# Kernel tuning notes

Hardware: AMD Instinct MI355X
Metric: run time of the kernel (lower is better)

The kernel has to match this reference:

```python
import jax, jax.numpy as jnp
import numpy as np

C = 64
DQK = C // 8  # query/key channels


def setup_inputs() -> dict:
    key = jax.random.key(0)
    ks = jax.random.split(key, 8)
    B, H, W = 4, 64, 64
    x = jax.random.normal(ks[0], (B, C, H, W), dtype=jnp.float32)
    # 1x1 conv weights stored as (out_ch, in_ch); biases as (out_ch,)
    wq = jax.random.normal(ks[1], (DQK, C), dtype=jnp.float32) * 0.05
    bq = jnp.zeros((DQK,), dtype=jnp.float32)
    wk = jax.random.normal(ks[2], (DQK, C), dtype=jnp.float32) * 0.05
    bk = jnp.zeros((DQK,), dtype=jnp.float32)
    wv = jax.random.normal(ks[3], (C, C), dtype=jnp.float32) * 0.05
    bv = jnp.zeros((C,), dtype=jnp.float32)
    gamma = jnp.zeros((1,), dtype=jnp.float32)
    return {"x": x, "wq": wq, "bq": bq, "wk": wk, "bk": bk,
            "wv": wv, "bv": bv, "gamma": gamma}


def reference(x, wq, bq, wk, bk, wv, bv, gamma):
    B, Cc, H, W = x.shape
    N = H * W
    xf = x.reshape(B, Cc, N)  # (B, C, N)
    # 1x1 convs == channel-wise matmuls
    q = jnp.einsum('oc,bcn->bon', wq, xf) + bq[None, :, None]  # (B, dqk, N)
    k = jnp.einsum('oc,bcn->bon', wk, xf) + bk[None, :, None]  # (B, dqk, N)
    v = jnp.einsum('oc,bcn->bon', wv, xf) + bv[None, :, None]  # (B, C, N)
    # qk = q^T k -> (B, N, N), softmax over last dim
    qk = jnp.einsum('bdn,bdm->bnm', q, k)
    attn = jax.nn.softmax(qk, axis=-1)
    # out = v @ attn^T : out[b,c,i] = sum_j v[b,c,j] * attn[b,i,j]
    out = jnp.einsum('bcj,bij->bci', v, attn)
    out = out.reshape(B, Cc, H, W)
    return gamma * out + x
```

## Files before the change

### kernel.cpp

```cpp
#include <hip/hip_runtime.h>
#include <cmath>

namespace {

constexpr int B = 4;
constexpr int C = 64;
constexpr int N = 4096;
constexpr float LOG2E = 1.4426950408889634f;

typedef __bf16 bf16x8 __attribute__((ext_vector_type(8)));
typedef float f32x16 __attribute__((ext_vector_type(16)));
typedef unsigned short u16;

union B8 {
  int4 i;
  bf16x8 h;
  unsigned int w[4];
};

__device__ inline u16 f2bf(float f) {
  unsigned int u = __float_as_uint(f);
  u += 0x7FFFu + ((u >> 16) & 1u);
  return (u16)(u >> 16);
}

__device__ inline unsigned int cvt_pk_bf16(float lo, float hi) {
  unsigned int r;
  asm("v_cvt_pk_bf16_f32 %0, %1, %2" : "=v"(r) : "v"(lo), "v"(hi));
  return r;
}

__device__ inline float exp2_fast(float x) {
#if __has_builtin(__builtin_amdgcn_exp2f)
  return __builtin_amdgcn_exp2f(x);
#else
  return exp2f(x);
#endif
}

__device__ __host__ inline int sigma4(int j) {
  return (j & 3) | ((j & 4) << 1) | ((j & 8) >> 1);
}

__global__ __launch_bounds__(256) void qkv_kernel(
    const float* __restrict__ x,
    const float* __restrict__ wq, const float* __restrict__ bq,
    const float* __restrict__ wk, const float* __restrict__ bk,
    const float* __restrict__ wv, const float* __restrict__ bv,
    u16* __restrict__ qt, u16* __restrict__ kt, u16* __restrict__ vo) {
  const int bid = blockIdx.x;
  const int xcd = bid & 7;
  const int b = xcd >> 1;
  const int cg = (bid >> 3) & 3;
  const int nt = (xcd & 1) * 32 + (bid >> 5);
  const int t = threadIdx.x;
  const int nn = t & 63;
  const int wid = __builtin_amdgcn_readfirstlane(t >> 6);
  const int n = nt * 64 + nn;
  const float* xb = x + (size_t)b * C * N + n;

  const int c0 = cg * 16 + wid * 4;
  float a0 = bv[c0], a1 = bv[c0 + 1], a2 = bv[c0 + 2], a3 = bv[c0 + 3];

  if (cg == 0) {
    const int o0 = wid * 2;
    float qa0 = bq[o0], qa1 = bq[o0 + 1];
    float ka0 = bk[o0], ka1 = bk[o0 + 1];
    #pragma unroll 8
    for (int c = 0; c < C; ++c) {
      const float xv = xb[(size_t)c * N];
      a0 = fmaf(wv[(c0 + 0) * C + c], xv, a0);
      a1 = fmaf(wv[(c0 + 1) * C + c], xv, a1);
      a2 = fmaf(wv[(c0 + 2) * C + c], xv, a2);
      a3 = fmaf(wv[(c0 + 3) * C + c], xv, a3);
      qa0 = fmaf(wq[o0 * C + c], xv, qa0);
      qa1 = fmaf(wq[(o0 + 1) * C + c], xv, qa1);
      ka0 = fmaf(wk[o0 * C + c], xv, ka0);
      ka1 = fmaf(wk[(o0 + 1) * C + c], xv, ka1);
    }
    const unsigned int qw =
        (unsigned int)f2bf(qa0 * LOG2E) | ((unsigned int)f2bf(qa1 * LOG2E) << 16);
    const unsigned int kw =
        (unsigned int)f2bf(ka0) | ((unsigned int)f2bf(ka1) << 16);
    *reinterpret_cast<unsigned int*>(qt + ((size_t)b * N + n) * 8 + o0) = qw;
    *reinterpret_cast<unsigned int*>(kt + ((size_t)b * N + n) * 8 + o0) = kw;
  } else {
    #pragma unroll 8
    for (int c = 0; c < C; ++c) {
      const float xv = xb[(size_t)c * N];
      a0 = fmaf(wv[(c0 + 0) * C + c], xv, a0);
      a1 = fmaf(wv[(c0 + 1) * C + c], xv, a1);
      a2 = fmaf(wv[(c0 + 2) * C + c], xv, a2);
      a3 = fmaf(wv[(c0 + 3) * C + c], xv, a3);
    }
  }

  const int sj = sigma4(n & 15);
  const size_t tb = ((size_t)b * (N / 16) + (n >> 4)) * (C * 16) + sj;
  vo[tb + (size_t)(c0 + 0) * 16] = f2bf(a0);
  vo[tb + (size_t)(c0 + 1) * 16] = f2bf(a1);
  vo[tb + (size_t)(c0 + 2) * 16] = f2bf(a2);
  vo[tb + (size_t)(c0 + 3) * 16] = f2bf(a3);
}

__global__ __launch_bounds__(512, 4) void attn_kernel(
    const u16* __restrict__ qt, const u16* __restrict__ kt,
    const u16* __restrict__ vv, const float* __restrict__ x,
    const float* __restrict__ gamma, float* __restrict__ out) {
  const int bid = blockIdx.x;
  const int xcd = bid & 7;
  const int b = xcd >> 1;
  const int i0 = ((xcd & 1) * 64 + (bid >> 3)) * 32;
  const int t = threadIdx.x;
  const int lane = t & 63;
  const int w = __builtin_amdgcn_readfirstlane(t >> 6);
  const int il = lane & 31;
  const int hi = lane >> 5;

  __shared__ float l_lds[8][32];
  __shared__ u16 o_lds[8][32][66];

  B8 qf;
  if (hi == 0)
    qf.i = *reinterpret_cast<const int4*>(qt + ((size_t)b * N + i0 + il) * 8);
  else
    qf.i = make_int4(0, 0, 0, 0);

  const u16* kbase = kt + (size_t)b * N * 8 + ((size_t)w * 512 + il) * 8;
  const u16* vbase = vv + (size_t)b * (N / 16) * (C * 16) + il * 16 + hi * 8;

  f32x16 accA, accB, zero16;
  #pragma unroll
  for (int r = 0; r < 16; ++r) { accA[r] = 0.f; accB[r] = 0.f; zero16[r] = 0.f; }
  float lrun = 0.f;

  B8 kfA, va0A, va1A, vb0A, vb1A;
  B8 kfB, va0B, va1B, vb0B, vb1B;

  auto LOAD = [&](int jt, B8& kf, B8& va0, B8& va1, B8& vb0, B8& vb1) {
    kf.i = *reinterpret_cast<const int4*>(kbase + jt * 256);
    const u16* vp = vbase + (size_t)((w * 512 + jt * 32) >> 4) * (C * 16);
    va0.i = *reinterpret_cast<const int4*>(vp);
    va1.i = *reinterpret_cast<const int4*>(vp + 1024);
    vb0.i = *reinterpret_cast<const int4*>(vp + 512);
    vb1.i = *reinterpret_cast<const int4*>(vp + 1536);
  };

  auto COMPUTE = [&](const B8& kf, const B8& va0, const B8& va1, const B8& vb0,
                     const B8& vb1) {
    f32x16 S = __builtin_amdgcn_mfma_f32_32x32x16_bf16(kf.h, qf.h, zero16, 0, 0, 0);
    float p[16];
    #pragma unroll
    for (int r = 0; r < 16; ++r) p[r] = exp2_fast(S[r]);
    const float t0 = (p[0] + p[1]) + (p[2] + p[3]);
    const float t1 = (p[4] + p[5]) + (p[6] + p[7]);
    const float t2 = (p[8] + p[9]) + (p[10] + p[11]);
    const float t3 = (p[12] + p[13]) + (p[14] + p[15]);
    lrun += (t0 + t1) + (t2 + t3);
    B8 pf0, pf1;
    pf0.w[0] = cvt_pk_bf16(p[0], p[1]);
    pf0.w[1] = cvt_pk_bf16(p[2], p[3]);
    pf0.w[2] = cvt_pk_bf16(p[4], p[5]);
    pf0.w[3] = cvt_pk_bf16(p[6], p[7]);
    pf1.w[0] = cvt_pk_bf16(p[8], p[9]);
    pf1.w[1] = cvt_pk_bf16(p[10], p[11]);
    pf1.w[2] = cvt_pk_bf16(p[12], p[13]);
    pf1.w[3] = cvt_pk_bf16(p[14], p[15]);
    accA = __builtin_amdgcn_mfma_f32_32x32x16_bf16(va0.h, pf0.h, accA, 0, 0, 0);
    accA = __builtin_amdgcn_mfma_f32_32x32x16_bf16(va1.h, pf1.h, accA, 0, 0, 0);
    accB = __builtin_amdgcn_mfma_f32_32x32x16_bf16(vb0.h, pf0.h, accB, 0, 0, 0);
    accB = __builtin_amdgcn_mfma_f32_32x32x16_bf16(vb1.h, pf1.h, accB, 0, 0, 0);
  };

  LOAD(0, kfA, va0A, va1A, vb0A, vb1A);
  #pragma unroll 1
  for (int it = 0; it < 8; ++it) {
    LOAD(2 * it + 1, kfB, va0B, va1B, vb0B, vb1B);
    COMPUTE(kfA, va0A, va1A, vb0A, vb1A);
    if (it < 7) LOAD(2 * it + 2, kfA, va0A, va1A, vb0A, vb1A);
    COMPUTE(kfB, va0B, va1B, vb0B, vb1B);
  }

  const float lw = lrun + __shfl_xor(lrun, 32);
  if (hi == 0) l_lds[w][il] = lw;
  #pragma unroll
  for (int r = 0; r < 16; r += 2) {
    const int c = (r & 3) + 8 * (r >> 2) + 4 * hi;
    *reinterpret_cast<unsigned int*>(&o_lds[w][il][c]) =
        cvt_pk_bf16(accA[r], accA[r + 1]);
    *reinterpret_cast<unsigned int*>(&o_lds[w][il][c + 32]) =
        cvt_pk_bf16(accB[r], accB[r + 1]);
  }
  __syncthreads();

  const int i = t & 31;
  float Li = 0.f;
  #pragma unroll
  for (int ww = 0; ww < 8; ++ww) Li += l_lds[ww][i];
  const float ginv = gamma[0] / Li;

  #pragma unroll
  for (int q4 = 0; q4 < 4; ++q4) {
    const int flat = t + q4 * 512;
    const int c = flat >> 5;
    float s = 0.f;
    #pragma unroll
    for (int ww = 0; ww < 8; ++ww)
      s += __uint_as_float((unsigned int)o_lds[ww][i][c] << 16);
    const size_t off = ((size_t)b * C + c) * N + i0 + i;
    out[off] = fmaf(ginv, s, x[off]);
  }
}

}

extern "C" void kernel_launch(void* const* d_in, const int* in_sizes, int n_in,
                              void* d_out, int out_size, void* d_ws, size_t ws_size,
                              hipStream_t stream) {
  const float* x     = (const float*)d_in[0];
  const float* wq    = (const float*)d_in[1];
  const float* bq    = (const float*)d_in[2];
  const float* wk    = (const float*)d_in[3];
  const float* bk    = (const float*)d_in[4];
  const float* wv    = (const float*)d_in[5];
  const float* bv    = (const float*)d_in[6];
  const float* gamma = (const float*)d_in[7];
  float* out = (float*)d_out;

  u16* qt = (u16*)d_ws;
  u16* kt = qt + (size_t)B * N * 8;
  u16* vo = kt + (size_t)B * N * 8;

  qkv_kernel<<<B * 64 * 4, 256, 0, stream>>>(x, wq, bq, wk, bk, wv, bv, qt, kt, vo);
  attn_kernel<<<B * (N / 32), 512, 0, stream>>>(qt, kt, vo, x, gamma, out);
}
```

Measured before the change: 29.52 us.

## Use packed f32 FMA/add and load V just-in-time in attention loop

The QKV projection loop now processes two input channels per step with v_pk_fma_f32 on two-lane accumulators, which are summed at the end. This halves the VALU instruction count and allows vector loads of weights. In the attention kernel, V fragments are loaded inside COMPUTE right after the score MFMA instead of being double-buffered a tile ahead, which cuts live registers. The softmax row-sum also uses packed adds. The risk is that V load latency is now exposed within each tile, hidden only by the exp work and by occupancy.

```diff
diff --git a/kernel.cpp b/kernel.cpp
--- a/kernel.cpp
+++ b/kernel.cpp
@@ -10,6 +10,7 @@
 
 typedef __bf16 bf16x8 __attribute__((ext_vector_type(8)));
 typedef float f32x16 __attribute__((ext_vector_type(16)));
+typedef float f32x2 __attribute__((ext_vector_type(2)));
 typedef unsigned short u16;
 
 union B8 {
@@ -27,6 +28,17 @@
 __device__ inline unsigned int cvt_pk_bf16(float lo, float hi) {
   unsigned int r;
   asm("v_cvt_pk_bf16_f32 %0, %1, %2" : "=v"(r) : "v"(lo), "v"(hi));
+  return r;
+}
+
+__device__ inline f32x2 pk_add(f32x2 a, f32x2 b) {
+  f32x2 r;
+  asm("v_pk_add_f32 %0, %1, %2" : "=v"(r) : "v"(a), "v"(b));
+  return r;
+}
+__device__ inline f32x2 pk_fma(f32x2 a, f32x2 b, f32x2 c) {
+  f32x2 r;
+  asm("v_pk_fma_f32 %0, %1, %2, %3" : "=v"(r) : "v"(a), "v"(b), "v"(c));
   return r;
 }
 
@@ -60,47 +72,48 @@
   const float* xb = x + (size_t)b * C * N + n;
 
   const int c0 = cg * 16 + wid * 4;
-  float a0 = bv[c0], a1 = bv[c0 + 1], a2 = bv[c0 + 2], a3 = bv[c0 + 3];
+  f32x2 av0 = {bv[c0], 0.f}, av1 = {bv[c0 + 1], 0.f};
+  f32x2 av2 = {bv[c0 + 2], 0.f}, av3 = {bv[c0 + 3], 0.f};
 
   if (cg == 0) {
     const int o0 = wid * 2;
-    float qa0 = bq[o0], qa1 = bq[o0 + 1];
-    float ka0 = bk[o0], ka1 = bk[o0 + 1];
+    f32x2 qa0 = {bq[o0], 0.f}, qa1 = {bq[o0 + 1], 0.f};
+    f32x2 ka0 = {bk[o0], 0.f}, ka1 = {bk[o0 + 1], 0.f};
     #pragma unroll 8
-    for (int c = 0; c < C; ++c) {
-      const float xv = xb[(size_t)c * N];
-      a0 = fmaf(wv[(c0 + 0) * C + c], xv, a0);
-      a1 = fmaf(wv[(c0 + 1) * C + c], xv, a1);
-      a2 = fmaf(wv[(c0 + 2) * C + c], xv, a2);
-      a3 = fmaf(wv[(c0 + 3) * C + c], xv, a3);
-      qa0 = fmaf(wq[o0 * C + c], xv, qa0);
-      qa1 = fmaf(wq[(o0 + 1) * C + c], xv, qa1);
-      ka0 = fmaf(wk[o0 * C + c], xv, ka0);
-      ka1 = fmaf(wk[(o0 + 1) * C + c], xv, ka1);
+    for (int c = 0; c < C; c += 2) {
+      const f32x2 xv = {xb[(size_t)c * N], xb[(size_t)(c + 1) * N]};
+      av0 = pk_fma(*(const f32x2*)&wv[(c0 + 0) * C + c], xv, av0);
+      av1 = pk_fma(*(const f32x2*)&wv[(c0 + 1) * C + c], xv, av1);
+      av2 = pk_fma(*(const f32x2*)&wv[(c0 + 2) * C + c], xv, av2);
+      av3 = pk_fma(*(const f32x2*)&wv[(c0 + 3) * C + c], xv, av3);
+      qa0 = pk_fma(*(const f32x2*)&wq[o0 * C + c], xv, qa0);
+      qa1 = pk_fma(*(const f32x2*)&wq[(o0 + 1) * C + c], xv, qa1);
+      ka0 = pk_fma(*(const f32x2*)&wk[o0 * C + c], xv, ka0);
+      ka1 = pk_fma(*(const f32x2*)&wk[(o0 + 1) * C + c], xv, ka1);
     }
-    const unsigned int qw =
-        (unsigned int)f2bf(qa0 * LOG2E) | ((unsigned int)f2bf(qa1 * LOG2E) << 16);
-    const unsigned int kw =
-        (unsigned int)f2bf(ka0) | ((unsigned int)f2bf(ka1) << 16);
+    const unsigned int qw = (unsigned int)f2bf((qa0.x + qa0.y) * LOG2E) |
+                            ((unsigned int)f2bf((qa1.x + qa1.y) * LOG2E) << 16);
+    const unsigned int kw = (unsigned int)f2bf(ka0.x + ka0.y) |
+                            ((unsigned int)f2bf(ka1.x + ka1.y) << 16);
     *reinterpret_cast<unsigned int*>(qt + ((size_t)b * N + n) * 8 + o0) = qw;
     *reinterpret_cast<unsigned int*>(kt + ((size_t)b * N + n) * 8 + o0) = kw;
   } else {
     #pragma unroll 8
-    for (int c = 0; c < C; ++c) {
-      const float xv = xb[(size_t)c * N];
-      a0 = fmaf(wv[(c0 + 0) * C + c], xv, a0);
-      a1 = fmaf(wv[(c0 + 1) * C + c], xv, a1);
-      a2 = fmaf(wv[(c0 + 2) * C + c], xv, a2);
-      a3 = fmaf(wv[(c0 + 3) * C + c], xv, a3);
+    for (int c = 0; c < C; c += 2) {
+      const f32x2 xv = {xb[(size_t)c * N], xb[(size_t)(c + 1) * N]};
+      av0 = pk_fma(*(const f32x2*)&wv[(c0 + 0) * C + c], xv, av0);
+      av1 = pk_fma(*(const f32x2*)&wv[(c0 + 1) * C + c], xv, av1);
+      av2 = pk_fma(*(const f32x2*)&wv[(c0 + 2) * C + c], xv, av2);
+      av3 = pk_fma(*(const f32x2*)&wv[(c0 + 3) * C + c], xv, av3);
     }
   }
 
   const int sj = sigma4(n & 15);
   const size_t tb = ((size_t)b * (N / 16) + (n >> 4)) * (C * 16) + sj;
-  vo[tb + (size_t)(c0 + 0) * 16] = f2bf(a0);
-  vo[tb + (size_t)(c0 + 1) * 16] = f2bf(a1);
-  vo[tb + (size_t)(c0 + 2) * 16] = f2bf(a2);
-  vo[tb + (size_t)(c0 + 3) * 16] = f2bf(a3);
+  vo[tb + (size_t)(c0 + 0) * 16] = f2bf(av0.x + av0.y);
+  vo[tb + (size_t)(c0 + 1) * 16] = f2bf(av1.x + av1.y);
+  vo[tb + (size_t)(c0 + 2) * 16] = f2bf(av2.x + av2.y);
+  vo[tb + (size_t)(c0 + 3) * 16] = f2bf(av3.x + av3.y);
 }
 
 __global__ __launch_bounds__(512, 4) void attn_kernel(
@@ -126,37 +139,36 @@
   else
     qf.i = make_int4(0, 0, 0, 0);
 
-  const u16* kbase = kt + (size_t)b * N * 8 + ((size_t)w * 512 + il) * 8;
-  const u16* vbase = vv + (size_t)b * (N / 16) * (C * 16) + il * 16 + hi * 8;
+  const u16* kcur = kt + (size_t)b * N * 8 + ((size_t)w * 512 + il) * 8;
+  const u16* vcur = vv + (size_t)b * (N / 16) * (C * 16) +
+                    (size_t)w * 32 * (C * 16) + il * 16 + hi * 8;
 
   f32x16 accA, accB, zero16;
   #pragma unroll
   for (int r = 0; r < 16; ++r) { accA[r] = 0.f; accB[r] = 0.f; zero16[r] = 0.f; }
-  float lrun = 0.f;
-
-  B8 kfA, va0A, va1A, vb0A, vb1A;
-  B8 kfB, va0B, va1B, vb0B, vb1B;
-
-  auto LOAD = [&](int jt, B8& kf, B8& va0, B8& va1, B8& vb0, B8& vb1) {
-    kf.i = *reinterpret_cast<const int4*>(kbase + jt * 256);
-    const u16* vp = vbase + (size_t)((w * 512 + jt * 32) >> 4) * (C * 16);
-    va0.i = *reinterpret_cast<const int4*>(vp);
-    va1.i = *reinterpret_cast<const int4*>(vp + 1024);
-    vb0.i = *reinterpret_cast<const int4*>(vp + 512);
-    vb1.i = *reinterpret_cast<const int4*>(vp + 1536);
-  };
-
-  auto COMPUTE = [&](const B8& kf, const B8& va0, const B8& va1, const B8& vb0,
-                     const B8& vb1) {
+  f32x2 lrun2 = {0.f, 0.f};
+
+  B8 kfA, kfB;
+
+  auto COMPUTE = [&](const B8& kf) {
     f32x16 S = __builtin_amdgcn_mfma_f32_32x32x16_bf16(kf.h, qf.h, zero16, 0, 0, 0);
+    B8 va0, va1, vb0, vb1;
+    va0.i = *reinterpret_cast<const int4*>(vcur);
+    va1.i = *reinterpret_cast<const int4*>(vcur + 1024);
+    vb0.i = *reinterpret_cast<const int4*>(vcur + 512);
+    vb1.i = *reinterpret_cast<const int4*>(vcur + 1536);
+    vcur += 2048;
     float p[16];
     #pragma unroll
     for (int r = 0; r < 16; ++r) p[r] = exp2_fast(S[r]);
-    const float t0 = (p[0] + p[1]) + (p[2] + p[3]);
-    const float t1 = (p[4] + p[5]) + (p[6] + p[7]);
-    const float t2 = (p[8] + p[9]) + (p[10] + p[11]);
-    const float t3 = (p[12] + p[13]) + (p[14] + p[15]);
-    lrun += (t0 + t1) + (t2 + t3);
+    const f32x2* u = reinterpret_cast<const f32x2*>(p);
+    f32x2 s0 = pk_add(u[0], u[1]);
+    f32x2 s1 = pk_add(u[2], u[3]);
+    f32x2 s2 = pk_add(u[4], u[5]);
+    f32x2 s3 = pk_add(u[6], u[7]);
+    s0 = pk_add(s0, s1);
+    s2 = pk_add(s2, s3);
+    lrun2 = pk_add(lrun2, pk_add(s0, s2));
     B8 pf0, pf1;
     pf0.w[0] = cvt_pk_bf16(p[0], p[1]);
     pf0.w[1] = cvt_pk_bf16(p[2], p[3]);
@@ -172,16 +184,22 @@
     accB = __builtin_amdgcn_mfma_f32_32x32x16_bf16(vb1.h, pf1.h, accB, 0, 0, 0);
   };
 
-  LOAD(0, kfA, va0A, va1A, vb0A, vb1A);
+  kfA.i = *reinterpret_cast<const int4*>(kcur);
+  kcur += 256;
   #pragma unroll 1
   for (int it = 0; it < 8; ++it) {
-    LOAD(2 * it + 1, kfB, va0B, va1B, vb0B, vb1B);
-    COMPUTE(kfA, va0A, va1A, vb0A, vb1A);
-    if (it < 7) LOAD(2 * it + 2, kfA, va0A, va1A, vb0A, vb1A);
-    COMPUTE(kfB, va0B, va1B, vb0B, vb1B);
-  }
-
-  const float lw = lrun + __shfl_xor(lrun, 32);
+    kfB.i = *reinterpret_cast<const int4*>(kcur);
+    kcur += 256;
+    COMPUTE(kfA);
+    if (it < 7) {
+      kfA.i = *reinterpret_cast<const int4*>(kcur);
+      kcur += 256;
+    }
+    COMPUTE(kfB);
+  }
+
+  const float lr = lrun2.x + lrun2.y;
+  const float lw = lr + __shfl_xor(lr, 32);
   if (hi == 0) l_lds[w][il] = lw;
   #pragma unroll
   for (int r = 0; r < 16; r += 2) {
```

Result: no change. 29.31 us (-0.7%).
